# Optimization experiments

Measured on AMD Instinct MI355X. Metric: run time of the kernel, lower is better.

Reference implementation:

```python
import jax, jax.numpy as jnp
import numpy as np

BASE = 10000.0

def positional_encoding(seq_len, dim, dtype=jnp.float32):
    # standard sinusoidal PE: pe[p, 2i] = sin(p / BASE^(2i/dim)), pe[p, 2i+1] = cos(...)
    pos = jnp.arange(seq_len, dtype=dtype)[:, None]            # [S,1]
    idx = jnp.arange(0, dim, 2, dtype=dtype)[None, :]          # [1,dim/2]
    ang = pos / jnp.power(BASE, idx / dim)                     # [S,dim/2]
    pe = jnp.zeros((seq_len, dim), dtype=dtype)
    pe = pe.at[:, 0::2].set(jnp.sin(ang)).at[:, 1::2].set(jnp.cos(ang))
    return pe

def setup_inputs() -> dict:
    key = jax.random.key(0)
    ks = jax.random.split(key, 5)
    B, S, H, D = 16, 2048, 128, 64
    x = jax.random.normal(ks[0], (B, S, H), dtype=jnp.float32)
    Wq = jax.random.normal(ks[1], (H, D), dtype=jnp.float32) * (H ** -0.5)
    Wk = jax.random.normal(ks[2], (H, D), dtype=jnp.float32) * (H ** -0.5)
    Wv = jax.random.normal(ks[3], (H, D), dtype=jnp.float32) * (H ** -0.5)
    Wf = jax.random.normal(ks[4], (D, 1), dtype=jnp.float32) * (D ** -0.5)
    bf = jnp.zeros((1,), dtype=jnp.float32)
    return {"x": x, "Wq": Wq, "Wk": Wk, "Wv": Wv, "Wf": Wf, "bf": bf}

def reference(x, Wq, Wk, Wv, Wf, bf):
    B, S, H = x.shape
    xp = x + positional_encoding(S, H, x.dtype)[None]          # add PE, broadcast over batch
    Q = jnp.einsum('bsh,hd->bsd', xp, Wq)
    K = jnp.einsum('bsh,hd->bsd', xp, Wk)
    V = jnp.einsum('bsh,hd->bsd', xp, Wv)
    D = K.shape[-1]
    scores = jnp.einsum('bqd,bkd->bqk', Q, K) / jnp.sqrt(jnp.asarray(D, x.dtype))
    # NOTE: softmax over dim=1 (the QUERY axis), per the original nn.Softmax(dim=1)
    attn = jax.nn.softmax(scores, axis=1)                      # [B,S,S]
    z = jnp.einsum('bqk,bkd->bqd', attn, V)                    # [B,S,D]
    out = (jnp.einsum('bsd,do->bso', z, Wf) + bf).squeeze(-1)  # [B,S]
    return out
```

## Files before the change

kernel.cpp:

```cpp
#include <hip/hip_runtime.h>
#include <hip/hip_bf16.h>
#include <math.h>

#define BATCH 16
#define SEQ   2048
#define HID   128
#define DIM   64

typedef __attribute__((ext_vector_type(8))) short bf16x8;
typedef __attribute__((ext_vector_type(4))) float f32x4;

#define QSCALE 0.18033688011112042f
#define C0_PE  0.07195578314043169f

static __device__ __forceinline__ ushort f2bf(float f) {
    union { float f; unsigned u; } v; v.f = f;
    unsigned r = v.u + 0x7FFFu + ((v.u >> 16) & 1u);
    return (ushort)(r >> 16);
}

static __device__ __forceinline__ float fast_exp2(float x) {
#if __has_builtin(__builtin_amdgcn_exp2f)
    return __builtin_amdgcn_exp2f(x);
#else
    return exp2f(x);
#endif
}

__global__ void k_prep(const float* __restrict__ Wq, const float* __restrict__ Wk,
                       const float* __restrict__ Wv, const float* __restrict__ Wf,
                       ushort* __restrict__ Wt, float* __restrict__ wvf) {
    const int tid = threadIdx.x;
    if (tid < HID) {
        float s = 0.f;
        #pragma unroll 8
        for (int d = 0; d < DIM; ++d) s += Wv[tid * DIM + d] * Wf[d];
        wvf[tid] = s;
    }
    for (int i = tid; i < 128 * 128; i += 256) {
        int col = i >> 7, k = i & 127;
        float v = (col < 64) ? Wq[k * DIM + col] * QSCALE : Wk[k * DIM + (col - 64)];
        Wt[i] = f2bf(v);
    }
}

__global__ __launch_bounds__(256) void k_qkv(
    const float* __restrict__ x, const ushort* __restrict__ Wt,
    const float* __restrict__ wvf, ushort* __restrict__ Qb,
    ushort* __restrict__ Kb, float* __restrict__ vf)
{
    const int tid  = threadIdx.x;
    const int wave = tid >> 6;
    const int lane = tid & 63;
    const int quad = lane >> 4;
    const int col  = lane & 15;
    const int rowbase = blockIdx.x * 64 + wave * 16;
    const int grow = rowbase + col;
    const float pos = (float)(grow & (SEQ - 1));

    bf16x8 af[4];
    float vpart = 0.f;
    #pragma unroll
    for (int c = 0; c < 4; ++c) {
        const float* xp = x + (size_t)grow * HID + quad * 8 + c * 32;
        float4 v0 = *(const float4*)(xp);
        float4 v1 = *(const float4*)(xp + 4);
        float t[8] = {v0.x, v0.y, v0.z, v0.w, v1.x, v1.y, v1.z, v1.w};
        #pragma unroll
        for (int jp = 0; jp < 4; ++jp) {
            int h = quad * 8 + c * 32 + jp * 2;
            float ang = pos * __expf(-(float)h * C0_PE);
            t[jp * 2]     += __sinf(ang);
            t[jp * 2 + 1] += __cosf(ang);
        }
        const float* wp = wvf + quad * 8 + c * 32;
        float4 w0 = *(const float4*)(wp);
        float4 w1 = *(const float4*)(wp + 4);
        vpart += t[0] * w0.x + t[1] * w0.y + t[2] * w0.z + t[3] * w0.w +
                 t[4] * w1.x + t[5] * w1.y + t[6] * w1.z + t[7] * w1.w;
        short* ap = (short*)&af[c];
        #pragma unroll
        for (int j = 0; j < 8; ++j) ap[j] = (short)f2bf(t[j]);
    }

    vpart += __shfl_xor(vpart, 16);
    vpart += __shfl_xor(vpart, 32);
    if (quad == 0) vf[grow] = vpart;

    #pragma unroll
    for (int t = 0; t < 8; ++t) {
        const ushort* wrow = Wt + (size_t)(t * 16 + col) * 128 + quad * 8;
        f32x4 acc = {0.f, 0.f, 0.f, 0.f};
        #pragma unroll
        for (int c = 0; c < 4; ++c) {
            bf16x8 bfr = *(const bf16x8*)(wrow + c * 32);
            acc = __builtin_amdgcn_mfma_f32_16x16x32_bf16(af[c], bfr, acc, 0, 0, 0);
        }
        const int cb = (t & 3) * 16 + col;
        ushort* dst = (t < 4) ? Qb : Kb;
        const int r0 = rowbase + quad * 4;
        #pragma unroll
        for (int r = 0; r < 4; ++r)
            dst[(size_t)(r0 + r) * DIM + cb] = f2bf(acc[r]);
    }
}

__global__ __launch_bounds__(512) void k_attn(
    const ushort* __restrict__ Qb, const ushort* __restrict__ Kb,
    const float* __restrict__ vf, const float* __restrict__ bfp,
    float* __restrict__ outp)
{
    const int b    = blockIdx.y;
    const int k0   = blockIdx.x * 64;
    const int tid  = threadIdx.x;
    const int wave = tid >> 6;
    const int lane = tid & 63;
    const int quad = lane >> 4;
    const int col  = lane & 15;

    __shared__ float sl[8][64];
    __shared__ float wcol[64];

    bf16x8 kf[4][2];
    {
        const ushort* Kbase = Kb + ((size_t)(b * SEQ + k0)) * DIM;
        #pragma unroll
        for (int t = 0; t < 4; ++t)
            #pragma unroll
            for (int c = 0; c < 2; ++c)
                kf[t][c] = *(const bf16x8*)(Kbase + (size_t)(t * 16 + col) * DIM + quad * 8 + c * 32);
    }

    const ushort* Qstart = Qb + ((size_t)(b * SEQ + wave * 256 + col)) * DIM + quad * 8;

    float l[4] = {0.f, 0.f, 0.f, 0.f};
    {
        const ushort* Qrow = Qstart;
        for (int qi = 0; qi < 16; ++qi) {
            bf16x8 a0 = *(const bf16x8*)(Qrow);
            bf16x8 a1 = *(const bf16x8*)(Qrow + 32);
            Qrow += 16 * DIM;
            #pragma unroll
            for (int t = 0; t < 4; ++t) {
                f32x4 acc = {0.f, 0.f, 0.f, 0.f};
                acc = __builtin_amdgcn_mfma_f32_16x16x32_bf16(a0, kf[t][0], acc, 0, 0, 0);
                acc = __builtin_amdgcn_mfma_f32_16x16x32_bf16(a1, kf[t][1], acc, 0, 0, 0);
                l[t] += fast_exp2(acc.x) + fast_exp2(acc.y) +
                        fast_exp2(acc.z) + fast_exp2(acc.w);
            }
        }
    }
    #pragma unroll
    for (int t = 0; t < 4; ++t) {
        l[t] += __shfl_xor(l[t], 16);
        l[t] += __shfl_xor(l[t], 32);
    }
    if (quad == 0) {
        #pragma unroll
        for (int t = 0; t < 4; ++t) sl[wave][t * 16 + col] = l[t];
    }
    __syncthreads();
    if (tid < 64) {
        float ll = 0.f;
        #pragma unroll
        for (int w = 0; w < 8; ++w) ll += sl[w][tid];
        wcol[tid] = vf[(size_t)b * SEQ + k0 + tid] / ll;
    }
    __syncthreads();

    const float bias = bfp[0] * (1.0f / (SEQ / 64));
    float wreg[4];
    #pragma unroll
    for (int t = 0; t < 4; ++t) wreg[t] = wcol[t * 16 + col];

    {
        const ushort* Qrow = Qstart;
        float* outb = outp + (size_t)b * SEQ;
        for (int qi = 0; qi < 16; ++qi) {
            bf16x8 a0 = *(const bf16x8*)(Qrow);
            bf16x8 a1 = *(const bf16x8*)(Qrow + 32);
            Qrow += 16 * DIM;
            float rs[4] = {0.f, 0.f, 0.f, 0.f};
            #pragma unroll
            for (int t = 0; t < 4; ++t) {
                f32x4 acc = {0.f, 0.f, 0.f, 0.f};
                acc = __builtin_amdgcn_mfma_f32_16x16x32_bf16(a0, kf[t][0], acc, 0, 0, 0);
                acc = __builtin_amdgcn_mfma_f32_16x16x32_bf16(a1, kf[t][1], acc, 0, 0, 0);
                #pragma unroll
                for (int r = 0; r < 4; ++r)
                    rs[r] += fast_exp2(acc[r]) * wreg[t];
            }
            #pragma unroll
            for (int r = 0; r < 4; ++r) {
                float v = rs[r];
                v += __shfl_xor(v, 1); v += __shfl_xor(v, 2);
                v += __shfl_xor(v, 4); v += __shfl_xor(v, 8);
                rs[r] = v;
            }
            if (col == 0) {
                const int qrow = wave * 256 + qi * 16 + quad * 4;
                #pragma unroll
                for (int r = 0; r < 4; ++r)
                    atomicAdd(&outb[qrow + r], rs[r] + bias);
            }
        }
    }
}

extern "C" void kernel_launch(void* const* d_in, const int* in_sizes, int n_in,
                              void* d_out, int out_size, void* d_ws, size_t ws_size,
                              hipStream_t stream) {
    (void)in_sizes; (void)n_in; (void)ws_size;
    const float* x  = (const float*)d_in[0];
    const float* Wq = (const float*)d_in[1];
    const float* Wk = (const float*)d_in[2];
    const float* Wv = (const float*)d_in[3];
    const float* Wf = (const float*)d_in[4];
    const float* bf = (const float*)d_in[5];
    float* outp = (float*)d_out;

    float*  wvf = (float*)d_ws;
    float*  vf  = wvf + 256;
    ushort* Wt  = (ushort*)(vf + (size_t)BATCH * SEQ);
    ushort* Qb  = Wt + 128 * 128;
    ushort* Kb  = Qb + (size_t)BATCH * SEQ * DIM;

    hipMemsetAsync(d_out, 0, (size_t)out_size * sizeof(float), stream);
    k_prep<<<1, 256, 0, stream>>>(Wq, Wk, Wv, Wf, Wt, wvf);
    k_qkv<<<BATCH * SEQ / 64, 256, 0, stream>>>(x, Wt, wvf, Qb, Kb, vf);
    k_attn<<<dim3(SEQ / 64, BATCH), 512, 0, stream>>>(Qb, Kb, vf, bf, outp);
}
```

Baseline: 138.2 us.

## Fuse weight prep into QKV kernel and swap MFMA operand order for cheaper reductions

Removes the single-block prep kernel and has every QKV block build the transposed bf16 Q/K weights and the Wv·Wf vector in padded shared memory. This saves one launch and its serial dependency, but each block now redoes the weight transform. The MFMA operand order is swapped in both kernels so each lane holds one row's outputs. That allows vectorized ushort4 Q/K stores and replaces the 4-step shuffle reduction per query row in the attention second pass with a 2-step one, with one atomic per lane instead of four per col-0 lane. The first pass now keeps 16 partial sums and reduces them once at the end.

```diff
diff --git a/kernel.cpp b/kernel.cpp
--- a/kernel.cpp
+++ b/kernel.cpp
@@ -6,6 +6,7 @@
 #define SEQ   2048
 #define HID   128
 #define DIM   64
+#define WTP   136
 
 typedef __attribute__((ext_vector_type(8))) short bf16x8;
 typedef __attribute__((ext_vector_type(4))) float f32x4;
@@ -27,33 +28,34 @@
 #endif
 }
 
-__global__ void k_prep(const float* __restrict__ Wq, const float* __restrict__ Wk,
-                       const float* __restrict__ Wv, const float* __restrict__ Wf,
-                       ushort* __restrict__ Wt, float* __restrict__ wvf) {
-    const int tid = threadIdx.x;
-    if (tid < HID) {
-        float s = 0.f;
-        #pragma unroll 8
-        for (int d = 0; d < DIM; ++d) s += Wv[tid * DIM + d] * Wf[d];
-        wvf[tid] = s;
-    }
-    for (int i = tid; i < 128 * 128; i += 256) {
-        int col = i >> 7, k = i & 127;
-        float v = (col < 64) ? Wq[k * DIM + col] * QSCALE : Wk[k * DIM + (col - 64)];
-        Wt[i] = f2bf(v);
-    }
-}
-
 __global__ __launch_bounds__(256) void k_qkv(
-    const float* __restrict__ x, const ushort* __restrict__ Wt,
-    const float* __restrict__ wvf, ushort* __restrict__ Qb,
+    const float* __restrict__ x, const float* __restrict__ Wq,
+    const float* __restrict__ Wk, const float* __restrict__ Wv,
+    const float* __restrict__ Wf, ushort* __restrict__ Qb,
     ushort* __restrict__ Kb, float* __restrict__ vf)
 {
+    __shared__ ushort Wt[128 * WTP];
+    __shared__ float  wvl[HID];
+
     const int tid  = threadIdx.x;
     const int wave = tid >> 6;
     const int lane = tid & 63;
     const int quad = lane >> 4;
     const int col  = lane & 15;
+
+    if (tid < HID) {
+        float s = 0.f;
+        #pragma unroll 8
+        for (int d = 0; d < DIM; ++d) s += Wv[tid * DIM + d] * Wf[d];
+        wvl[tid] = s;
+    }
+    for (int i = tid; i < 128 * 128; i += 256) {
+        int k = i >> 7, oc = i & 127;
+        float v = (oc < 64) ? Wq[k * DIM + oc] * QSCALE : Wk[k * DIM + (oc - 64)];
+        Wt[oc * WTP + k] = f2bf(v);
+    }
+    __syncthreads();
+
     const int rowbase = blockIdx.x * 64 + wave * 16;
     const int grow = rowbase + col;
     const float pos = (float)(grow & (SEQ - 1));
@@ -73,11 +75,9 @@
             t[jp * 2]     += __sinf(ang);
             t[jp * 2 + 1] += __cosf(ang);
         }
-        const float* wp = wvf + quad * 8 + c * 32;
-        float4 w0 = *(const float4*)(wp);
-        float4 w1 = *(const float4*)(wp + 4);
-        vpart += t[0] * w0.x + t[1] * w0.y + t[2] * w0.z + t[3] * w0.w +
-                 t[4] * w1.x + t[5] * w1.y + t[6] * w1.z + t[7] * w1.w;
+        const float* wp = wvl + quad * 8 + c * 32;
+        vpart += t[0] * wp[0] + t[1] * wp[1] + t[2] * wp[2] + t[3] * wp[3] +
+                 t[4] * wp[4] + t[5] * wp[5] + t[6] * wp[6] + t[7] * wp[7];
         short* ap = (short*)&af[c];
         #pragma unroll
         for (int j = 0; j < 8; ++j) ap[j] = (short)f2bf(t[j]);
@@ -89,19 +89,16 @@
 
     #pragma unroll
     for (int t = 0; t < 8; ++t) {
-        const ushort* wrow = Wt + (size_t)(t * 16 + col) * 128 + quad * 8;
+        const ushort* wrow = Wt + (size_t)(t * 16 + col) * WTP + quad * 8;
         f32x4 acc = {0.f, 0.f, 0.f, 0.f};
         #pragma unroll
         for (int c = 0; c < 4; ++c) {
-            bf16x8 bfr = *(const bf16x8*)(wrow + c * 32);
-            acc = __builtin_amdgcn_mfma_f32_16x16x32_bf16(af[c], bfr, acc, 0, 0, 0);
-        }
-        const int cb = (t & 3) * 16 + col;
+            bf16x8 wfr = *(const bf16x8*)(wrow + c * 32);
+            acc = __builtin_amdgcn_mfma_f32_16x16x32_bf16(wfr, af[c], acc, 0, 0, 0);
+        }
+        ushort4 o = {f2bf(acc.x), f2bf(acc.y), f2bf(acc.z), f2bf(acc.w)};
         ushort* dst = (t < 4) ? Qb : Kb;
-        const int r0 = rowbase + quad * 4;
-        #pragma unroll
-        for (int r = 0; r < 4; ++r)
-            dst[(size_t)(r0 + r) * DIM + cb] = f2bf(acc[r]);
+        *(ushort4*)&dst[(size_t)grow * DIM + (t & 3) * 16 + quad * 4] = o;
     }
 }
 
@@ -133,31 +130,39 @@
 
     const ushort* Qstart = Qb + ((size_t)(b * SEQ + wave * 256 + col)) * DIM + quad * 8;
 
-    float l[4] = {0.f, 0.f, 0.f, 0.f};
+    float l[4][4] = {};
     {
         const ushort* Qrow = Qstart;
         for (int qi = 0; qi < 16; ++qi) {
-            bf16x8 a0 = *(const bf16x8*)(Qrow);
-            bf16x8 a1 = *(const bf16x8*)(Qrow + 32);
+            bf16x8 q0 = *(const bf16x8*)(Qrow);
+            bf16x8 q1 = *(const bf16x8*)(Qrow + 32);
             Qrow += 16 * DIM;
             #pragma unroll
             for (int t = 0; t < 4; ++t) {
                 f32x4 acc = {0.f, 0.f, 0.f, 0.f};
-                acc = __builtin_amdgcn_mfma_f32_16x16x32_bf16(a0, kf[t][0], acc, 0, 0, 0);
-                acc = __builtin_amdgcn_mfma_f32_16x16x32_bf16(a1, kf[t][1], acc, 0, 0, 0);
-                l[t] += fast_exp2(acc.x) + fast_exp2(acc.y) +
-                        fast_exp2(acc.z) + fast_exp2(acc.w);
+                acc = __builtin_amdgcn_mfma_f32_16x16x32_bf16(kf[t][0], q0, acc, 0, 0, 0);
+                acc = __builtin_amdgcn_mfma_f32_16x16x32_bf16(kf[t][1], q1, acc, 0, 0, 0);
+                #pragma unroll
+                for (int r = 0; r < 4; ++r)
+                    l[t][r] += fast_exp2(acc[r]);
             }
         }
     }
     #pragma unroll
-    for (int t = 0; t < 4; ++t) {
-        l[t] += __shfl_xor(l[t], 16);
-        l[t] += __shfl_xor(l[t], 32);
-    }
-    if (quad == 0) {
-        #pragma unroll
-        for (int t = 0; t < 4; ++t) sl[wave][t * 16 + col] = l[t];
+    for (int t = 0; t < 4; ++t)
+        #pragma unroll
+        for (int r = 0; r < 4; ++r) {
+            float v = l[t][r];
+            v += __shfl_xor(v, 1); v += __shfl_xor(v, 2);
+            v += __shfl_xor(v, 4); v += __shfl_xor(v, 8);
+            l[t][r] = v;
+        }
+    if (col == 0) {
+        #pragma unroll
+        for (int t = 0; t < 4; ++t)
+            #pragma unroll
+            for (int r = 0; r < 4; ++r)
+                sl[wave][t * 16 + quad * 4 + r] = l[t][r];
     }
     __syncthreads();
     if (tid < 64) {
@@ -168,41 +173,35 @@
     }
     __syncthreads();
 
+    float wreg[4][4];
+    #pragma unroll
+    for (int t = 0; t < 4; ++t)
+        #pragma unroll
+        for (int r = 0; r < 4; ++r)
+            wreg[t][r] = wcol[t * 16 + quad * 4 + r];
+
     const float bias = bfp[0] * (1.0f / (SEQ / 64));
-    float wreg[4];
-    #pragma unroll
-    for (int t = 0; t < 4; ++t) wreg[t] = wcol[t * 16 + col];
-
+    float* outb = outp + (size_t)b * SEQ;
     {
         const ushort* Qrow = Qstart;
-        float* outb = outp + (size_t)b * SEQ;
         for (int qi = 0; qi < 16; ++qi) {
-            bf16x8 a0 = *(const bf16x8*)(Qrow);
-            bf16x8 a1 = *(const bf16x8*)(Qrow + 32);
+            bf16x8 q0 = *(const bf16x8*)(Qrow);
+            bf16x8 q1 = *(const bf16x8*)(Qrow + 32);
             Qrow += 16 * DIM;
-            float rs[4] = {0.f, 0.f, 0.f, 0.f};
+            float rs = 0.f;
             #pragma unroll
             for (int t = 0; t < 4; ++t) {
                 f32x4 acc = {0.f, 0.f, 0.f, 0.f};
-                acc = __builtin_amdgcn_mfma_f32_16x16x32_bf16(a0, kf[t][0], acc, 0, 0, 0);
-                acc = __builtin_amdgcn_mfma_f32_16x16x32_bf16(a1, kf[t][1], acc, 0, 0, 0);
+                acc = __builtin_amdgcn_mfma_f32_16x16x32_bf16(kf[t][0], q0, acc, 0, 0, 0);
+                acc = __builtin_amdgcn_mfma_f32_16x16x32_bf16(kf[t][1], q1, acc, 0, 0, 0);
                 #pragma unroll
                 for (int r = 0; r < 4; ++r)
-                    rs[r] += fast_exp2(acc[r]) * wreg[t];
+                    rs += fast_exp2(acc[r]) * wreg[t][r];
             }
-            #pragma unroll
-            for (int r = 0; r < 4; ++r) {
-                float v = rs[r];
-                v += __shfl_xor(v, 1); v += __shfl_xor(v, 2);
-                v += __shfl_xor(v, 4); v += __shfl_xor(v, 8);
-                rs[r] = v;
-            }
-            if (col == 0) {
-                const int qrow = wave * 256 + qi * 16 + quad * 4;
-                #pragma unroll
-                for (int r = 0; r < 4; ++r)
-                    atomicAdd(&outb[qrow + r], rs[r] + bias);
-            }
+            rs += __shfl_xor(rs, 16);
+            rs += __shfl_xor(rs, 32);
+            if (quad == 0)
+                atomicAdd(&outb[wave * 256 + qi * 16 + col], rs + bias);
         }
     }
 }
@@ -219,14 +218,11 @@
     const float* bf = (const float*)d_in[5];
     float* outp = (float*)d_out;
 
-    float*  wvf = (float*)d_ws;
-    float*  vf  = wvf + 256;
-    ushort* Wt  = (ushort*)(vf + (size_t)BATCH * SEQ);
-    ushort* Qb  = Wt + 128 * 128;
-    ushort* Kb  = Qb + (size_t)BATCH * SEQ * DIM;
+    float*  vf = (float*)d_ws;
+    ushort* Qb = (ushort*)(vf + (size_t)BATCH * SEQ);
+    ushort* Kb = Qb + (size_t)BATCH * SEQ * DIM;
 
     hipMemsetAsync(d_out, 0, (size_t)out_size * sizeof(float), stream);
-    k_prep<<<1, 256, 0, stream>>>(Wq, Wk, Wv, Wf, Wt, wvf);
-    k_qkv<<<BATCH * SEQ / 64, 256, 0, stream>>>(x, Wt, wvf, Qb, Kb, vf);
+    k_qkv<<<BATCH * SEQ / 64, 256, 0, stream>>>(x, Wq, Wk, Wv, Wf, Qb, Kb, vf);
     k_attn<<<dim3(SEQ / 64, BATCH), 512, 0, stream>>>(Qb, Kb, vf, bf, outp);
 }
```

After: 139.5 us. Within noise of the previous version (+1.0%).
